# Optimization experiments

Hardware: AMD Instinct MI355X
Metric: run time of the kernel (lower is better)

The kernel has to match this reference:

```python
import jax, jax.numpy as jnp
import numpy as np

# Static module configuration (from init_kwargs)
BL, BS = 256, 256            # batch_size_large, batch_size_small
R_LARGE, R_SMALL = 64, 16
R_MULT = R_LARGE // R_SMALL  # 4: each large adapter split into 4 rank-16 slices
D = 4096
N_SPLIT = 32 * R_MULT + 64   # 192 splitted adapters
LB = BL * R_MULT + BS        # 1280 lora rows


def setup_inputs() -> dict:
    key = jax.random.key(0)
    k1, k2, k3, k4, k5 = jax.random.split(key, 5)
    x = jax.random.normal(k1, (BL + BS, 1, D), dtype=jnp.float16)
    lora_A = jax.random.normal(k2, (N_SPLIT, D, R_SMALL), dtype=jnp.float16) * jnp.float16(0.02)
    lora_B = jax.random.normal(k3, (N_SPLIT, R_SMALL, D), dtype=jnp.float16) * jnp.float16(0.02)
    xids = jax.random.randint(k4, (LB,), 0, BL + BS, dtype=jnp.int32)
    wids = jax.random.randint(k5, (LB,), 0, N_SPLIT, dtype=jnp.int32)
    return {"x": x, "lora_A": lora_A, "lora_B": lora_B, "xids": xids, "wids": wids}


def reference(x, lora_A, lora_B, xids, wids):
    # gather token activations and per-row rank-16 adapter slices
    xg = x[xids]                 # [LB, 1, D]
    Ag = lora_A[wids]            # [LB, D, r]
    Bg = lora_B[wids]            # [LB, r, D]
    h = jnp.einsum('bod,bdr->bor', xg, Ag)          # [LB, 1, r]
    y = jnp.einsum('bor,brd->bod', h, Bg) * jnp.float16(2.0)  # [LB, 1, D]
    # split+sum: first BL groups of R_MULT rows are summed (keepdims),
    # last BS rows pass through -> equivalent to a segment-sum.
    seg = jnp.concatenate([jnp.repeat(jnp.arange(BL), R_MULT), BL + jnp.arange(BS)])
    z = jax.ops.segment_sum(y[:, 0, :], seg, num_segments=BL + BS)  # [BL+BS, D]
    return z[:, None, :]         # [batch_size, 1, D]
```

## Files before the change

### kernel.cpp

```cpp
#include <hip/hip_runtime.h>
#include <stdint.h>

typedef __attribute__((ext_vector_type(4))) float float4v;

#define D 4096
#define R 16
#define NW 192
#define LB 1280
#define NBL 256
#define MAXB 32
#define TQ 8
#define DQ 1024

__global__ __launch_bounds__(256) void h_kernel(
    const float* __restrict__ x,
    const float* __restrict__ A,
    const int* __restrict__ xids,
    const int* __restrict__ wids,
    float* __restrict__ hpart)
{
    const int w = blockIdx.x >> 2;
    const int q = blockIdx.x & 3;
    const int t = threadIdx.x;
    const int lane = t & 63;
    const int wave = t >> 6;
    const int g = t >> 2;
    const int c = t & 3;

    __shared__ int list[MAXB], xidl[MAXB];
    __shared__ int cnt;
    __shared__ float xs[TQ][DQ];
    __shared__ float hws[TQ][4][R];

    if (t == 0) cnt = 0;
    __syncthreads();
    for (int i = t; i < LB; i += 256)
        if (wids[i] == w) { int p = atomicAdd(&cnt, 1); if (p < MAXB) list[p] = i; }
    __syncthreads();
    const int n = cnt > MAXB ? MAXB : cnt;
    if (n == 0) return;
    if (t < n) xidl[t] = xids[list[t]];

    const float4v* af = (const float4v*)(A + ((size_t)w * D + q * DQ) * R);
    float4v a[4][4];
    #pragma unroll
    for (int k = 0; k < 4; ++k)
        #pragma unroll
        for (int j = 0; j < 4; ++j)
            a[k][j] = af[16 * g + 1024 * k + 4 * j + c];

    for (int tb = 0; tb < n; tb += TQ) {
        const int T = min(TQ, n - tb);
        __syncthreads();
        for (int i = 0; i < T; ++i) {
            float4v v = *(const float4v*)(x + (size_t)xidl[tb + i] * D + q * DQ + 4 * t);
            *(float4v*)&xs[i][4 * t] = v;
        }
        __syncthreads();

        for (int i = 0; i < T; ++i) {
            float4v xv[4];
            #pragma unroll
            for (int k = 0; k < 4; ++k)
                xv[k] = *(const float4v*)&xs[i][4 * g + 256 * k];
            float h0 = 0.f, h1 = 0.f, h2 = 0.f, h3 = 0.f;
            #pragma unroll
            for (int k = 0; k < 4; ++k)
                #pragma unroll
                for (int j = 0; j < 4; ++j) {
                    const float xd = xv[k][j];
                    h0 += xd * a[k][j][0];
                    h1 += xd * a[k][j][1];
                    h2 += xd * a[k][j][2];
                    h3 += xd * a[k][j][3];
                }
            #pragma unroll
            for (int off = 4; off <= 32; off <<= 1) {
                h0 += __shfl_xor(h0, off, 64);
                h1 += __shfl_xor(h1, off, 64);
                h2 += __shfl_xor(h2, off, 64);
                h3 += __shfl_xor(h3, off, 64);
            }
            if (lane < 4) {
                float4v hv = {h0, h1, h2, h3};
                *(float4v*)&hws[i][wave][4 * lane] = hv;
            }
        }
        __syncthreads();
        for (int idx = t; idx < T * R; idx += 256) {
            const int i = idx >> 4, r = idx & 15;
            const float s = hws[i][0][r] + hws[i][1][r] + hws[i][2][r] + hws[i][3][r];
            hpart[(size_t)list[tb + i] * 64 + q * 16 + r] = s;
        }
    }
}

__global__ __launch_bounds__(256) void y_kernel(
    const float* __restrict__ B,
    const int* __restrict__ wids,
    const float* __restrict__ hpart,
    float* __restrict__ ybuf,
    float* __restrict__ out)
{
    const int w = blockIdx.x >> 2;
    const int q = blockIdx.x & 3;
    const int t = threadIdx.x;

    __shared__ int list[MAXB];
    __shared__ int cnt;
    __shared__ float hl[MAXB][R];

    if (t == 0) cnt = 0;
    __syncthreads();
    for (int i = t; i < LB; i += 256)
        if (wids[i] == w) { int p = atomicAdd(&cnt, 1); if (p < MAXB) list[p] = i; }
    __syncthreads();
    const int n = cnt > MAXB ? MAXB : cnt;
    if (n == 0) return;

    const float* Bw = B + (size_t)w * R * D + q * DQ + 4 * t;
    float4v breg[R];
    #pragma unroll
    for (int r = 0; r < R; ++r) breg[r] = *(const float4v*)(Bw + (size_t)r * D);

    for (int idx = t; idx < n * R; idx += 256) {
        const int i = idx >> 4, r = idx & 15;
        const float* hp = hpart + (size_t)list[i] * 64 + r;
        hl[i][r] = (hp[0] + hp[16]) + (hp[32] + hp[48]);
    }
    __syncthreads();

    for (int i = 0; i < n; ++i) {
        const int b = list[i];
        float4v acc = {0.f, 0.f, 0.f, 0.f};
        #pragma unroll
        for (int r = 0; r < R; ++r) {
            const float hr = hl[i][r];
            acc[0] += hr * breg[r][0];
            acc[1] += hr * breg[r][1];
            acc[2] += hr * breg[r][2];
            acc[3] += hr * breg[r][3];
        }
        #pragma unroll
        for (int k = 0; k < 4; ++k) acc[k] *= 2.0f;

        if (b < NBL * 4) {
            *(float4v*)(ybuf + (size_t)b * D + q * DQ + 4 * t) = acc;
        } else {
            *(float4v*)(out + (size_t)(NBL + (b - NBL * 4)) * D + q * DQ + 4 * t) = acc;
        }
    }
}

__global__ __launch_bounds__(256) void sum4_kernel(
    const float* __restrict__ ybuf,
    float* __restrict__ out)
{
    const int o = blockIdx.x >> 2;
    const int q = blockIdx.x & 3;
    const int col = q * DQ + 4 * threadIdx.x;
    const float* y0 = ybuf + (size_t)(4 * o) * D + col;
    float4v v0 = *(const float4v*)(y0);
    float4v v1 = *(const float4v*)(y0 + D);
    float4v v2 = *(const float4v*)(y0 + 2 * D);
    float4v v3 = *(const float4v*)(y0 + 3 * D);
    float4v s;
    #pragma unroll
    for (int k = 0; k < 4; ++k) s[k] = (v0[k] + v1[k]) + (v2[k] + v3[k]);
    *(float4v*)(out + (size_t)o * D + col) = s;
}

extern "C" void kernel_launch(void* const* d_in, const int* in_sizes, int n_in,
                              void* d_out, int out_size, void* d_ws, size_t ws_size,
                              hipStream_t stream) {
    const float* x    = (const float*)d_in[0];
    const float* A    = (const float*)d_in[1];
    const float* B    = (const float*)d_in[2];
    const int*   xids = (const int*)d_in[3];
    const int*   wids = (const int*)d_in[4];
    float*       out  = (float*)d_out;

    float* hpart = (float*)d_ws;
    float* ybuf  = hpart + (size_t)LB * 64;

    hipLaunchKernelGGL(h_kernel, dim3(NW * 4), dim3(256), 0, stream,
                       x, A, xids, wids, hpart);
    hipLaunchKernelGGL(y_kernel, dim3(NW * 4), dim3(256), 0, stream,
                       B, wids, hpart, ybuf, out);
    hipLaunchKernelGGL(sum4_kernel, dim3(NBL * 4), dim3(256), 0, stream,
                       ybuf, out);
}
```

Before: 158.2 us.

## Fuse three LoRA kernels into one persistent kernel with grid barriers

Merges the h, y and segment-sum kernels into a single 768-block launch that synchronises with atomic-counter grid barriers. The B-slice register loads are issued before the first barrier so they overlap with waiting. This removes two kernel launch gaps but requires every block to be co-resident, and adds a memset launch plus barrier spin costs. Intermediate stores become relaxed atomic stores, and the ybuf writes are split from vector stores into scalar stores.

```diff
diff --git a/kernel.cpp b/kernel.cpp
--- a/kernel.cpp
+++ b/kernel.cpp
@@ -11,13 +11,31 @@
 #define MAXB 32
 #define TQ 8
 #define DQ 1024
+#define GRID (NW * 4)
 
-__global__ __launch_bounds__(256) void h_kernel(
+__device__ __forceinline__ void grid_barrier(int* ctr) {
+    __syncthreads();
+    if (threadIdx.x == 0) {
+        __threadfence();
+        atomicAdd(ctr, 1);
+        while (__hip_atomic_load(ctr, __ATOMIC_ACQUIRE,
+                                 __HIP_MEMORY_SCOPE_AGENT) < GRID)
+            __builtin_amdgcn_s_sleep(8);
+        __threadfence();
+    }
+    __syncthreads();
+}
+
+__global__ __launch_bounds__(256, 4) void fused_all(
     const float* __restrict__ x,
     const float* __restrict__ A,
+    const float* __restrict__ B,
     const int* __restrict__ xids,
     const int* __restrict__ wids,
-    float* __restrict__ hpart)
+    int* __restrict__ bar,
+    float* __restrict__ hpart,
+    float* __restrict__ ybuf,
+    float* __restrict__ out)
 {
     const int w = blockIdx.x >> 2;
     const int q = blockIdx.x & 3;
@@ -31,83 +49,6 @@
     __shared__ int cnt;
     __shared__ float xs[TQ][DQ];
     __shared__ float hws[TQ][4][R];
-
-    if (t == 0) cnt = 0;
-    __syncthreads();
-    for (int i = t; i < LB; i += 256)
-        if (wids[i] == w) { int p = atomicAdd(&cnt, 1); if (p < MAXB) list[p] = i; }
-    __syncthreads();
-    const int n = cnt > MAXB ? MAXB : cnt;
-    if (n == 0) return;
-    if (t < n) xidl[t] = xids[list[t]];
-
-    const float4v* af = (const float4v*)(A + ((size_t)w * D + q * DQ) * R);
-    float4v a[4][4];
-    #pragma unroll
-    for (int k = 0; k < 4; ++k)
-        #pragma unroll
-        for (int j = 0; j < 4; ++j)
-            a[k][j] = af[16 * g + 1024 * k + 4 * j + c];
-
-    for (int tb = 0; tb < n; tb += TQ) {
-        const int T = min(TQ, n - tb);
-        __syncthreads();
-        for (int i = 0; i < T; ++i) {
-            float4v v = *(const float4v*)(x + (size_t)xidl[tb + i] * D + q * DQ + 4 * t);
-            *(float4v*)&xs[i][4 * t] = v;
-        }
-        __syncthreads();
-
-        for (int i = 0; i < T; ++i) {
-            float4v xv[4];
-            #pragma unroll
-            for (int k = 0; k < 4; ++k)
-                xv[k] = *(const float4v*)&xs[i][4 * g + 256 * k];
-            float h0 = 0.f, h1 = 0.f, h2 = 0.f, h3 = 0.f;
-            #pragma unroll
-            for (int k = 0; k < 4; ++k)
-                #pragma unroll
-                for (int j = 0; j < 4; ++j) {
-                    const float xd = xv[k][j];
-                    h0 += xd * a[k][j][0];
-                    h1 += xd * a[k][j][1];
-                    h2 += xd * a[k][j][2];
-                    h3 += xd * a[k][j][3];
-                }
-            #pragma unroll
-            for (int off = 4; off <= 32; off <<= 1) {
-                h0 += __shfl_xor(h0, off, 64);
-                h1 += __shfl_xor(h1, off, 64);
-                h2 += __shfl_xor(h2, off, 64);
-                h3 += __shfl_xor(h3, off, 64);
-            }
-            if (lane < 4) {
-                float4v hv = {h0, h1, h2, h3};
-                *(float4v*)&hws[i][wave][4 * lane] = hv;
-            }
-        }
-        __syncthreads();
-        for (int idx = t; idx < T * R; idx += 256) {
-            const int i = idx >> 4, r = idx & 15;
-            const float s = hws[i][0][r] + hws[i][1][r] + hws[i][2][r] + hws[i][3][r];
-            hpart[(size_t)list[tb + i] * 64 + q * 16 + r] = s;
-        }
-    }
-}
-
-__global__ __launch_bounds__(256) void y_kernel(
-    const float* __restrict__ B,
-    const int* __restrict__ wids,
-    const float* __restrict__ hpart,
-    float* __restrict__ ybuf,
-    float* __restrict__ out)
-{
-    const int w = blockIdx.x >> 2;
-    const int q = blockIdx.x & 3;
-    const int t = threadIdx.x;
-
-    __shared__ int list[MAXB];
-    __shared__ int cnt;
     __shared__ float hl[MAXB][R];
 
     if (t == 0) cnt = 0;
@@ -116,58 +57,124 @@
         if (wids[i] == w) { int p = atomicAdd(&cnt, 1); if (p < MAXB) list[p] = i; }
     __syncthreads();
     const int n = cnt > MAXB ? MAXB : cnt;
-    if (n == 0) return;
-
-    const float* Bw = B + (size_t)w * R * D + q * DQ + 4 * t;
-    float4v breg[R];
-    #pragma unroll
-    for (int r = 0; r < R; ++r) breg[r] = *(const float4v*)(Bw + (size_t)r * D);
-
-    for (int idx = t; idx < n * R; idx += 256) {
-        const int i = idx >> 4, r = idx & 15;
-        const float* hp = hpart + (size_t)list[i] * 64 + r;
-        hl[i][r] = (hp[0] + hp[16]) + (hp[32] + hp[48]);
-    }
+    if (t < n) xidl[t] = xids[list[t]];
     __syncthreads();
 
-    for (int i = 0; i < n; ++i) {
-        const int b = list[i];
-        float4v acc = {0.f, 0.f, 0.f, 0.f};
+    if (n > 0) {
+        const float4v* af = (const float4v*)(A + ((size_t)w * D + q * DQ) * R);
+        float4v a[4][4];
         #pragma unroll
-        for (int r = 0; r < R; ++r) {
-            const float hr = hl[i][r];
-            acc[0] += hr * breg[r][0];
-            acc[1] += hr * breg[r][1];
-            acc[2] += hr * breg[r][2];
-            acc[3] += hr * breg[r][3];
-        }
-        #pragma unroll
-        for (int k = 0; k < 4; ++k) acc[k] *= 2.0f;
+        for (int k = 0; k < 4; ++k)
+            #pragma unroll
+            for (int j = 0; j < 4; ++j)
+                a[k][j] = af[16 * g + 1024 * k + 4 * j + c];
 
-        if (b < NBL * 4) {
-            *(float4v*)(ybuf + (size_t)b * D + q * DQ + 4 * t) = acc;
-        } else {
-            *(float4v*)(out + (size_t)(NBL + (b - NBL * 4)) * D + q * DQ + 4 * t) = acc;
+        for (int tb = 0; tb < n; tb += TQ) {
+            const int T = min(TQ, n - tb);
+            __syncthreads();
+            for (int i = 0; i < T; ++i) {
+                float4v v = *(const float4v*)(x + (size_t)xidl[tb + i] * D + q * DQ + 4 * t);
+                *(float4v*)&xs[i][4 * t] = v;
+            }
+            __syncthreads();
+
+            for (int i = 0; i < T; ++i) {
+                float4v xv[4];
+                #pragma unroll
+                for (int k = 0; k < 4; ++k)
+                    xv[k] = *(const float4v*)&xs[i][4 * g + 256 * k];
+                float h0 = 0.f, h1 = 0.f, h2 = 0.f, h3 = 0.f;
+                #pragma unroll
+                for (int k = 0; k < 4; ++k)
+                    #pragma unroll
+                    for (int j = 0; j < 4; ++j) {
+                        const float xd = xv[k][j];
+                        h0 += xd * a[k][j][0];
+                        h1 += xd * a[k][j][1];
+                        h2 += xd * a[k][j][2];
+                        h3 += xd * a[k][j][3];
+                    }
+                #pragma unroll
+                for (int off = 4; off <= 32; off <<= 1) {
+                    h0 += __shfl_xor(h0, off, 64);
+                    h1 += __shfl_xor(h1, off, 64);
+                    h2 += __shfl_xor(h2, off, 64);
+                    h3 += __shfl_xor(h3, off, 64);
+                }
+                if (lane < 4) {
+                    float4v hv = {h0, h1, h2, h3};
+                    *(float4v*)&hws[i][wave][4 * lane] = hv;
+                }
+            }
+            __syncthreads();
+            for (int idx = t; idx < T * R; idx += 256) {
+                const int i = idx >> 4, r = idx & 15;
+                const float s = hws[i][0][r] + hws[i][1][r] + hws[i][2][r] + hws[i][3][r];
+                __hip_atomic_store(&hpart[(size_t)list[tb + i] * 64 + q * 16 + r],
+                                   s, __ATOMIC_RELAXED, __HIP_MEMORY_SCOPE_AGENT);
+            }
         }
     }
-}
 
-__global__ __launch_bounds__(256) void sum4_kernel(
-    const float* __restrict__ ybuf,
-    float* __restrict__ out)
-{
-    const int o = blockIdx.x >> 2;
-    const int q = blockIdx.x & 3;
-    const int col = q * DQ + 4 * threadIdx.x;
-    const float* y0 = ybuf + (size_t)(4 * o) * D + col;
-    float4v v0 = *(const float4v*)(y0);
-    float4v v1 = *(const float4v*)(y0 + D);
-    float4v v2 = *(const float4v*)(y0 + 2 * D);
-    float4v v3 = *(const float4v*)(y0 + 3 * D);
-    float4v s;
-    #pragma unroll
-    for (int k = 0; k < 4; ++k) s[k] = (v0[k] + v1[k]) + (v2[k] + v3[k]);
-    *(float4v*)(out + (size_t)o * D + col) = s;
+    float4v breg[R];
+    if (n > 0) {
+        const float* Bw = B + (size_t)w * R * D + q * DQ + 4 * t;
+        #pragma unroll
+        for (int r = 0; r < R; ++r) breg[r] = *(const float4v*)(Bw + (size_t)r * D);
+    }
+
+    grid_barrier(&bar[0]);
+
+    if (n > 0) {
+        for (int idx = t; idx < n * R; idx += 256) {
+            const int i = idx >> 4, r = idx & 15;
+            const float* hp = hpart + (size_t)list[i] * 64 + r;
+            hl[i][r] = (hp[0] + hp[16]) + (hp[32] + hp[48]);
+        }
+        __syncthreads();
+
+        for (int i = 0; i < n; ++i) {
+            const int b = list[i];
+            float4v acc = {0.f, 0.f, 0.f, 0.f};
+            #pragma unroll
+            for (int r = 0; r < R; ++r) {
+                const float hr = hl[i][r];
+                acc[0] += hr * breg[r][0];
+                acc[1] += hr * breg[r][1];
+                acc[2] += hr * breg[r][2];
+                acc[3] += hr * breg[r][3];
+            }
+            #pragma unroll
+            for (int k = 0; k < 4; ++k) acc[k] *= 2.0f;
+
+            if (b < NBL * 4) {
+                float* yb = ybuf + (size_t)b * D + q * DQ + 4 * t;
+                #pragma unroll
+                for (int k = 0; k < 4; ++k)
+                    __hip_atomic_store(yb + k, acc[k], __ATOMIC_RELAXED,
+                                       __HIP_MEMORY_SCOPE_AGENT);
+            } else {
+                *(float4v*)(out + (size_t)(NBL + (b - NBL * 4)) * D + q * DQ + 4 * t) = acc;
+            }
+        }
+    }
+
+    grid_barrier(&bar[1]);
+
+    for (int ch = blockIdx.x; ch < NBL * 4; ch += GRID) {
+        const int o = ch >> 2;
+        const int cq = ch & 3;
+        const int col = cq * DQ + 4 * t;
+        const float* y0 = ybuf + (size_t)(4 * o) * D + col;
+        float4v v0 = *(const float4v*)(y0);
+        float4v v1 = *(const float4v*)(y0 + D);
+        float4v v2 = *(const float4v*)(y0 + 2 * D);
+        float4v v3 = *(const float4v*)(y0 + 3 * D);
+        float4v s;
+        #pragma unroll
+        for (int k = 0; k < 4; ++k) s[k] = (v0[k] + v1[k]) + (v2[k] + v3[k]);
+        *(float4v*)(out + (size_t)o * D + col) = s;
+    }
 }
 
 extern "C" void kernel_launch(void* const* d_in, const int* in_sizes, int n_in,
@@ -180,13 +187,11 @@
     const int*   wids = (const int*)d_in[4];
     float*       out  = (float*)d_out;
 
-    float* hpart = (float*)d_ws;
+    int*   bar   = (int*)d_ws;
+    float* hpart = (float*)d_ws + 64;
     float* ybuf  = hpart + (size_t)LB * 64;
 
-    hipLaunchKernelGGL(h_kernel, dim3(NW * 4), dim3(256), 0, stream,
-                       x, A, xids, wids, hpart);
-    hipLaunchKernelGGL(y_kernel, dim3(NW * 4), dim3(256), 0, stream,
-                       B, wids, hpart, ybuf, out);
-    hipLaunchKernelGGL(sum4_kernel, dim3(NBL * 4), dim3(256), 0, stream,
-                       ybuf, out);
+    hipMemsetAsync(bar, 0, 2 * sizeof(int), stream);
+    hipLaunchKernelGGL(fused_all, dim3(GRID), dim3(256), 0, stream,
+                       x, A, B, xids, wids, bar, hpart, ybuf, out);
 }
```

After: 428.6 us. 171% more time.
